# Performance work log

Measured on AMD Instinct MI355X. Metric: run time of the kernel, lower is better.

## Reference

```python
import jax, jax.numpy as jnp
import numpy as np


def setup_inputs() -> dict:
    key = jax.random.key(0)
    k1, k2, k3, k4, k5 = jax.random.split(key, 5)
    b, n, L, D, m = 8, 8192, 512, 128, 16
    x = jax.random.normal(k1, (b, n, L), dtype=jnp.float32)
    # attention MLP: Linear(L->D, no bias), Tanh, Linear(D->1, no bias)
    W1 = jax.random.normal(k2, (L, D), dtype=jnp.float32) / np.sqrt(L).astype(np.float32)
    W2 = jax.random.normal(k3, (D, 1), dtype=jnp.float32) / np.sqrt(D).astype(np.float32)
    batched_image_ids = jax.random.randint(k4, (b, n), 0, m)  # which image each packed token belongs to
    key_pad_mask = jax.random.bernoulli(k5, 0.1, (b, n))      # True = padding token
    return {"x": x, "W1": W1, "W2": W2,
            "batched_image_ids": batched_image_ids,
            "key_pad_mask": key_pad_mask,
            "max_queries": 16}


def reference(x, W1, W2, batched_image_ids, key_pad_mask, max_queries):
    # Attention scores per token: tanh(x W1) W2 -> [b, n, 1]
    A = jnp.tanh(x @ W1) @ W2
    A = jnp.swapaxes(A, -1, -2)  # [b, 1, n]
    b, n, d = x.shape
    # Per-image pooling mask: token j contributes to query i iff its image id == i and not padded
    image_id_arange = jnp.arange(max_queries)                                    # [m]
    attn_pool_mask = (image_id_arange[None, :, None] == batched_image_ids[:, None, :])
    attn_pool_mask = attn_pool_mask & (~key_pad_mask)[:, None, :]                # [b, m, n]
    neg = -jnp.finfo(A.dtype).max
    A = jnp.where(attn_pool_mask, jnp.broadcast_to(A, (b, max_queries, n)), neg)
    A = jax.nn.softmax(A, axis=-1)                                               # [b, m, n]
    out = jnp.einsum('bmn,bnd->bmd', A, x)                                       # pooled per image
    # num_images == max_queries for every bag -> is_images selects everything
    out = out.reshape(b * max_queries, d)
    return out
```

## Files before the change

kernel.cpp:

```cpp
#include <hip/hip_runtime.h>
#include <hip/hip_bf16.h>
#include <cstdint>
#include <cstddef>

typedef __attribute__((ext_vector_type(8))) short bf16x8;
typedef __attribute__((ext_vector_type(4))) float f32x4;

#define BATCH 8
#define NTOK 8192
#define LDIM 512
#define DDIM 128
#define NQ 16
#define NSEG 8
#define SEGLEN (NTOK / NSEG)

static __device__ __forceinline__ short f2bf(float f) {
  uint32_t u = __float_as_uint(f);
  uint32_t r = u + 0x7fffu + ((u >> 16) & 1u);
  return (short)(r >> 16);
}

static __device__ __forceinline__ bf16x8 cvt8(float4 a, float4 b) {
  bf16x8 o;
  o[0] = f2bf(a.x); o[1] = f2bf(a.y); o[2] = f2bf(a.z); o[3] = f2bf(a.w);
  o[4] = f2bf(b.x); o[5] = f2bf(b.y); o[6] = f2bf(b.z); o[7] = f2bf(b.w);
  return o;
}

static __device__ __forceinline__ unsigned int flipf(float v) {
  unsigned int u = __float_as_uint(v);
  return (u & 0x80000000u) ? ~u : (u | 0x80000000u);
}
static __device__ __forceinline__ float unflipf(unsigned int u) {
  return __uint_as_float((u & 0x80000000u) ? (u & 0x7fffffffu) : ~u);
}

static __device__ __forceinline__ bool is_pad(const void* pad, int byteFlag, int j) {
  return byteFlag ? (((const unsigned char*)pad)[j] != 0)
                  : (((const int*)pad)[j] != 0);
}

__global__ __launch_bounds__(256) void k0_wfrag(const float* __restrict__ W1,
                                                short* __restrict__ wfrag,
                                                const unsigned int* __restrict__ pad_raw,
                                                int* __restrict__ flag,
                                                unsigned int* __restrict__ gmax) {
  int tid = blockIdx.x * blockDim.x + threadIdx.x;
  if (tid < 16 * 8 * 64) {
    int l = tid & 63;
    int t = (tid >> 6) & 7;
    int c = tid >> 9;
    int kbase = c * 32 + (l >> 4) * 8;
    int col = t * 16 + (l & 15);
    bf16x8 frag;
#pragma unroll
    for (int i = 0; i < 8; ++i) frag[i] = f2bf(W1[(size_t)(kbase + i) * DDIM + col]);
    ((bf16x8*)wfrag)[tid] = frag;
  }
  if (blockIdx.x == 0) {
    if (threadIdx.x < 128) gmax[threadIdx.x] = 0u;
    int any_gt1 = 0;
    for (int i = threadIdx.x; i < 16384; i += 256)
      if (pad_raw[i] > 1u) any_gt1 = 1;
    unsigned long long m = __ballot(any_gt1);
    __shared__ int s[4];
    if ((threadIdx.x & 63) == 0) s[threadIdx.x >> 6] = (m != 0ull) ? 1 : 0;
    __syncthreads();
    if (threadIdx.x == 0) flag[0] = (s[0] | s[1] | s[2] | s[3]);
  }
}

__global__ __launch_bounds__(512, 6) void k1_scores(const float* __restrict__ x,
                                                    const short* __restrict__ wfrag,
                                                    const float* __restrict__ W2,
                                                    const int* __restrict__ ids,
                                                    const void* __restrict__ pad,
                                                    const int* __restrict__ flag,
                                                    float* __restrict__ A,
                                                    unsigned int* __restrict__ gmax) {
  __shared__ short ldsw[16384];
  __shared__ unsigned int qmax[16];
  const int tid = threadIdx.x, wave = tid >> 6, lane = tid & 63;
  const int rowBase = blockIdx.x * 128 + wave * 16;
  const int b = rowBase >> 13;
  const float* xp = x + (size_t)(rowBase + (lane & 15)) * LDIM + ((lane >> 4) * 8);
  if (tid < 16) qmax[tid] = 0u;

#define STAGE(qd)                                                                             \
  {                                                                                           \
    const unsigned int* src_ = (const unsigned int*)wfrag + (qd) * 8192;                      \
    _Pragma("unroll")                                                                         \
    for (int i = 0; i < 4; ++i) {                                                             \
      __builtin_amdgcn_global_load_lds(                                                       \
          (const __attribute__((address_space(1))) unsigned int*)(src_ + (i * 512 + tid) * 4),\
          (__attribute__((address_space(3))) unsigned int*)&ldsw[(i * 512 + wave * 64) * 8],  \
          16, 0, 0);                                                                          \
    }                                                                                         \
  }

#define ALOAD(dst, c)                                  \
  {                                                    \
    dst[0] = *(const float4*)(xp + (c) * 32);          \
    dst[1] = *(const float4*)(xp + (c) * 32 + 4);      \
  }

  f32x4 acc[8];
#pragma unroll
  for (int t = 0; t < 8; ++t) acc[t] = (f32x4){0.f, 0.f, 0.f, 0.f};
  float4 avbuf[2][2];

  STAGE(0);
  ALOAD(avbuf[0], 0);
  ALOAD(avbuf[1], 1);
  __syncthreads();

#pragma unroll
  for (int qd = 0; qd < 4; ++qd) {
#pragma unroll
    for (int cc = 0; cc < 4; ++cc) {
      const int c = qd * 4 + cc;
      bf16x8 af = cvt8(avbuf[c & 1][0], avbuf[c & 1][1]);
      if (c < 14) ALOAD(avbuf[c & 1], c + 2);
#pragma unroll
      for (int t = 0; t < 8; ++t) {
        bf16x8 bfr = *(const bf16x8*)&ldsw[((cc * 8 + t) * 64 + lane) * 8];
        acc[t] = __builtin_amdgcn_mfma_f32_16x16x32_bf16(af, bfr, acc[t], 0, 0, 0);
      }
    }
    if (qd < 3) {
      __syncthreads();
      STAGE(qd + 1);
      __syncthreads();
    }
  }
#undef STAGE
#undef ALOAD

  float w2v[8];
#pragma unroll
  for (int t = 0; t < 8; ++t) w2v[t] = W2[t * 16 + (lane & 15)];
  const int bfl = flag[0];
  float asum[4] = {0.f, 0.f, 0.f, 0.f};
#pragma unroll
  for (int t = 0; t < 8; ++t) {
#pragma unroll
    for (int r = 0; r < 4; ++r) {
      float h = 1.f - 2.f / (__expf(2.f * acc[t][r]) + 1.f);
      asum[r] += h * w2v[t];
    }
  }
#pragma unroll
  for (int m = 1; m < 16; m <<= 1) {
#pragma unroll
    for (int r = 0; r < 4; ++r) asum[r] += __shfl_xor(asum[r], m, 64);
  }
  if ((lane & 15) == 0) {
    int rb = rowBase + (lane >> 4) * 4;
#pragma unroll
    for (int r = 0; r < 4; ++r) {
      int row = rb + r;
      float v = asum[r];
      A[row] = v;
      if (!is_pad(pad, bfl, row)) atomicMax(&qmax[ids[row]], flipf(v));
    }
  }
  __syncthreads();
  if (tid < 16 && qmax[tid] != 0u) atomicMax(&gmax[(b << 4) + tid], qmax[tid]);
}

__global__ __launch_bounds__(256) void k3_pool(const float* __restrict__ x,
                                               const float* __restrict__ A,
                                               const int* __restrict__ ids,
                                               const void* __restrict__ pad,
                                               const int* __restrict__ flag,
                                               const unsigned int* __restrict__ gmax,
                                               float* __restrict__ partial,
                                               float* __restrict__ wsum) {
  int blk = blockIdx.x;
  int s = blk & 7, q = (blk >> 3) & 15, b = blk >> 7;
  int wave = threadIdx.x >> 6, lane = threadIdx.x & 63;
  int bfl = flag[0];
  __shared__ float w_u[1024];
  __shared__ unsigned short j_u[1024];
  __shared__ int cnt[4];
  __shared__ float wred[4];

  unsigned int mraw = gmax[(b << 4) + q];
  float mx = (mraw == 0u) ? 0.f : unflipf(mraw);
  const int base = b * NTOK;
  const int tokBase = s * SEGLEN + wave * 256;

  int myCnt = 0;
#pragma unroll
  for (int g = 0; g < 4; ++g) {
    int j = tokBase + g * 64 + lane;
    bool mem = (ids[base + j] == q) && !is_pad(pad, bfl, base + j);
    myCnt += __popcll(__ballot(mem));
  }
  if (lane == 0) cnt[wave] = myCnt;
  __syncthreads();

  int wpos = 0;
#pragma unroll
  for (int w = 0; w < 4; ++w) if (w < wave) wpos += cnt[w];
  const int total = cnt[0] + cnt[1] + cnt[2] + cnt[3];

  float wacc = 0.f;
#pragma unroll
  for (int g = 0; g < 4; ++g) {
    int j = tokBase + g * 64 + lane;
    bool mem = (ids[base + j] == q) && !is_pad(pad, bfl, base + j);
    float wt = mem ? __expf(A[base + j] - mx) : 0.f;
    wacc += wt;
    unsigned long long mask = __ballot(mem);
    if (mem) {
      int pos = wpos + __popcll(mask & ((1ull << lane) - 1ull));
      w_u[pos] = wt;
      j_u[pos] = (unsigned short)j;
    }
    wpos += __popcll(mask);
  }
#pragma unroll
  for (int m = 1; m < 64; m <<= 1) wacc += __shfl_xor(wacc, m, 64);
  if (lane == 0) wred[wave] = wacc;
  __syncthreads();

  int grp = threadIdx.x >> 7, ct = threadIdx.x & 127;
  int c0 = ct * 4;
  int half = (total + 1) >> 1;
  int e0 = grp ? half : 0;
  int e1 = grp ? total : half;
  float4 av = {0.f, 0.f, 0.f, 0.f};
  for (int e = e0; e < e1; ++e) {
    float wt = w_u[e];
    int j = j_u[e];
    float4 xr = *(const float4*)(x + (size_t)(base + j) * LDIM + c0);
    av.x += wt * xr.x; av.y += wt * xr.y; av.z += wt * xr.z; av.w += wt * xr.w;
  }
  *(float4*)(partial + ((size_t)(blk * 2 + grp)) * LDIM + c0) = av;
  if (threadIdx.x == 0) wsum[blk] = wred[0] + wred[1] + wred[2] + wred[3];
}

__global__ void k4_reduce(const float* __restrict__ partial, const float* __restrict__ wsum,
                          float* __restrict__ out) {
  int e = blockIdx.x * blockDim.x + threadIdx.x;
  if (e >= BATCH * NQ * LDIM) return;
  int bi = e >> 9, c = e & 511;
  float ps = 0.f, ws = 0.f;
#pragma unroll
  for (int t = 0; t < 16; ++t) ps += partial[(size_t)(bi * 16 + t) * LDIM + c];
#pragma unroll
  for (int t = 0; t < 8; ++t) ws += wsum[bi * 8 + t];
  out[e] = (ws > 0.f) ? (ps / ws) : 0.f;
}

extern "C" void kernel_launch(void* const* d_in, const int* in_sizes, int n_in,
                              void* d_out, int out_size, void* d_ws, size_t ws_size,
                              hipStream_t stream) {
  const float* x = (const float*)d_in[0];
  const float* W1 = (const float*)d_in[1];
  const float* W2 = (const float*)d_in[2];
  const int* ids = (const int*)d_in[3];
  const void* pad = d_in[4];
  float* out = (float*)d_out;

  char* ws = (char*)d_ws;
  short* wfrag = (short*)ws;
  float* A = (float*)(ws + 131072);
  unsigned int* gmax = (unsigned int*)(ws + 393216);
  float* wsum = (float*)(ws + 393728);
  int* flag = (int*)(ws + 397824);
  float* partial = (float*)(ws + 397952);

  hipLaunchKernelGGL(k0_wfrag, dim3(32), dim3(256), 0, stream,
                     W1, wfrag, (const unsigned int*)pad, flag, gmax);
  hipLaunchKernelGGL(k1_scores, dim3((BATCH * NTOK) / 128), dim3(512), 0, stream,
                     x, wfrag, W2, ids, pad, flag, A, gmax);
  hipLaunchKernelGGL(k3_pool, dim3(BATCH * NQ * NSEG), dim3(256), 0, stream,
                     x, A, ids, pad, flag, gmax, partial, wsum);
  hipLaunchKernelGGL(k4_reduce, dim3((BATCH * NQ * LDIM) / 256), dim3(256), 0, stream,
                     partial, wsum, out);
}
```

Before: 70.67 us.

## Fuse softmax-weighted pooling into score kernel, drop max pass and pool kernel

Computes exp of the attention score directly in the scores kernel and pools x rows of the same 128-token tile per image into per-block partials. This removes the separate pool kernel, so x is not read from memory a second time, and removes the global max atomics. The max subtraction is dropped, relying on the scores being bounded by the tanh. A larger partial buffer (16 per block) must now be written and reduced by a new reduce kernel.

New measurement: 91.90 us. 1.3x slower.

```diff
diff --git a/kernel.cpp b/kernel.cpp
--- a/kernel.cpp
+++ b/kernel.cpp
@@ -11,8 +11,6 @@
 #define LDIM 512
 #define DDIM 128
 #define NQ 16
-#define NSEG 8
-#define SEGLEN (NTOK / NSEG)
 
 static __device__ __forceinline__ short f2bf(float f) {
   uint32_t u = __float_as_uint(f);
@@ -27,14 +25,6 @@
   return o;
 }
 
-static __device__ __forceinline__ unsigned int flipf(float v) {
-  unsigned int u = __float_as_uint(v);
-  return (u & 0x80000000u) ? ~u : (u | 0x80000000u);
-}
-static __device__ __forceinline__ float unflipf(unsigned int u) {
-  return __uint_as_float((u & 0x80000000u) ? (u & 0x7fffffffu) : ~u);
-}
-
 static __device__ __forceinline__ bool is_pad(const void* pad, int byteFlag, int j) {
   return byteFlag ? (((const unsigned char*)pad)[j] != 0)
                   : (((const int*)pad)[j] != 0);
@@ -43,8 +33,7 @@
 __global__ __launch_bounds__(256) void k0_wfrag(const float* __restrict__ W1,
                                                 short* __restrict__ wfrag,
                                                 const unsigned int* __restrict__ pad_raw,
-                                                int* __restrict__ flag,
-                                                unsigned int* __restrict__ gmax) {
+                                                int* __restrict__ flag) {
   int tid = blockIdx.x * blockDim.x + threadIdx.x;
   if (tid < 16 * 8 * 64) {
     int l = tid & 63;
@@ -58,7 +47,6 @@
     ((bf16x8*)wfrag)[tid] = frag;
   }
   if (blockIdx.x == 0) {
-    if (threadIdx.x < 128) gmax[threadIdx.x] = 0u;
     int any_gt1 = 0;
     for (int i = threadIdx.x; i < 16384; i += 256)
       if (pad_raw[i] > 1u) any_gt1 = 1;
@@ -70,21 +58,22 @@
   }
 }
 
-__global__ __launch_bounds__(512, 6) void k1_scores(const float* __restrict__ x,
-                                                    const short* __restrict__ wfrag,
-                                                    const float* __restrict__ W2,
-                                                    const int* __restrict__ ids,
-                                                    const void* __restrict__ pad,
-                                                    const int* __restrict__ flag,
-                                                    float* __restrict__ A,
-                                                    unsigned int* __restrict__ gmax) {
+__global__ __launch_bounds__(512, 6) void k1_fused(const float* __restrict__ x,
+                                                   const short* __restrict__ wfrag,
+                                                   const float* __restrict__ W2,
+                                                   const int* __restrict__ ids,
+                                                   const void* __restrict__ pad,
+                                                   const int* __restrict__ flag,
+                                                   float* __restrict__ partial,
+                                                   float* __restrict__ wsum_p) {
   __shared__ short ldsw[16384];
-  __shared__ unsigned int qmax[16];
+  __shared__ float wt_l[128];
+  __shared__ int qq_l[128];
+  __shared__ int idx_l[128];
+  __shared__ int off_l[17];
   const int tid = threadIdx.x, wave = tid >> 6, lane = tid & 63;
   const int rowBase = blockIdx.x * 128 + wave * 16;
-  const int b = rowBase >> 13;
   const float* xp = x + (size_t)(rowBase + (lane & 15)) * LDIM + ((lane >> 4) * 8);
-  if (tid < 16) qmax[tid] = 0u;
 
 #define STAGE(qd)                                                                             \
   {                                                                                           \
@@ -155,103 +144,72 @@
     for (int r = 0; r < 4; ++r) asum[r] += __shfl_xor(asum[r], m, 64);
   }
   if ((lane & 15) == 0) {
-    int rb = rowBase + (lane >> 4) * 4;
 #pragma unroll
     for (int r = 0; r < 4; ++r) {
-      int row = rb + r;
-      float v = asum[r];
-      A[row] = v;
-      if (!is_pad(pad, bfl, row)) atomicMax(&qmax[ids[row]], flipf(v));
-    }
-  }
-  __syncthreads();
-  if (tid < 16 && qmax[tid] != 0u) atomicMax(&gmax[(b << 4) + tid], qmax[tid]);
-}
-
-__global__ __launch_bounds__(256) void k3_pool(const float* __restrict__ x,
-                                               const float* __restrict__ A,
-                                               const int* __restrict__ ids,
-                                               const void* __restrict__ pad,
-                                               const int* __restrict__ flag,
-                                               const unsigned int* __restrict__ gmax,
-                                               float* __restrict__ partial,
-                                               float* __restrict__ wsum) {
-  int blk = blockIdx.x;
-  int s = blk & 7, q = (blk >> 3) & 15, b = blk >> 7;
-  int wave = threadIdx.x >> 6, lane = threadIdx.x & 63;
-  int bfl = flag[0];
-  __shared__ float w_u[1024];
-  __shared__ unsigned short j_u[1024];
-  __shared__ int cnt[4];
-  __shared__ float wred[4];
-
-  unsigned int mraw = gmax[(b << 4) + q];
-  float mx = (mraw == 0u) ? 0.f : unflipf(mraw);
-  const int base = b * NTOK;
-  const int tokBase = s * SEGLEN + wave * 256;
-
-  int myCnt = 0;
-#pragma unroll
-  for (int g = 0; g < 4; ++g) {
-    int j = tokBase + g * 64 + lane;
-    bool mem = (ids[base + j] == q) && !is_pad(pad, bfl, base + j);
-    myCnt += __popcll(__ballot(mem));
-  }
-  if (lane == 0) cnt[wave] = myCnt;
-  __syncthreads();
-
-  int wpos = 0;
-#pragma unroll
-  for (int w = 0; w < 4; ++w) if (w < wave) wpos += cnt[w];
-  const int total = cnt[0] + cnt[1] + cnt[2] + cnt[3];
-
-  float wacc = 0.f;
-#pragma unroll
-  for (int g = 0; g < 4; ++g) {
-    int j = tokBase + g * 64 + lane;
-    bool mem = (ids[base + j] == q) && !is_pad(pad, bfl, base + j);
-    float wt = mem ? __expf(A[base + j] - mx) : 0.f;
-    wacc += wt;
-    unsigned long long mask = __ballot(mem);
-    if (mem) {
-      int pos = wpos + __popcll(mask & ((1ull << lane) - 1ull));
-      w_u[pos] = wt;
-      j_u[pos] = (unsigned short)j;
-    }
-    wpos += __popcll(mask);
-  }
-#pragma unroll
-  for (int m = 1; m < 64; m <<= 1) wacc += __shfl_xor(wacc, m, 64);
-  if (lane == 0) wred[wave] = wacc;
-  __syncthreads();
-
-  int grp = threadIdx.x >> 7, ct = threadIdx.x & 127;
-  int c0 = ct * 4;
-  int half = (total + 1) >> 1;
-  int e0 = grp ? half : 0;
-  int e1 = grp ? total : half;
-  float4 av = {0.f, 0.f, 0.f, 0.f};
-  for (int e = e0; e < e1; ++e) {
-    float wt = w_u[e];
-    int j = j_u[e];
-    float4 xr = *(const float4*)(x + (size_t)(base + j) * LDIM + c0);
-    av.x += wt * xr.x; av.y += wt * xr.y; av.z += wt * xr.z; av.w += wt * xr.w;
-  }
-  *(float4*)(partial + ((size_t)(blk * 2 + grp)) * LDIM + c0) = av;
-  if (threadIdx.x == 0) wsum[blk] = wred[0] + wred[1] + wred[2] + wred[3];
-}
-
-__global__ void k4_reduce(const float* __restrict__ partial, const float* __restrict__ wsum,
-                          float* __restrict__ out) {
-  int e = blockIdx.x * blockDim.x + threadIdx.x;
-  if (e >= BATCH * NQ * LDIM) return;
-  int bi = e >> 9, c = e & 511;
-  float ps = 0.f, ws = 0.f;
-#pragma unroll
-  for (int t = 0; t < 16; ++t) ps += partial[(size_t)(bi * 16 + t) * LDIM + c];
-#pragma unroll
-  for (int t = 0; t < 8; ++t) ws += wsum[bi * 8 + t];
-  out[e] = (ws > 0.f) ? (ps / ws) : 0.f;
+      int lr = wave * 16 + (lane >> 4) * 4 + r;
+      int row = blockIdx.x * 128 + lr;
+      wt_l[lr] = __expf(asum[r]);
+      qq_l[lr] = is_pad(pad, bfl, row) ? 16 : ids[row];
+    }
+  }
+  __syncthreads();
+
+  if (wave == 0) {
+    int q0 = qq_l[lane], q1 = qq_l[64 + lane];
+    unsigned long long below = (1ull << lane) - 1ull;
+    int pos = 0;
+    for (int q = 0; q < 16; ++q) {
+      if (lane == 0) off_l[q] = pos;
+      unsigned long long m0 = __ballot(q0 == q);
+      if (q0 == q) idx_l[pos + __popcll(m0 & below)] = lane;
+      int c0 = __popcll(m0);
+      unsigned long long m1 = __ballot(q1 == q);
+      if (q1 == q) idx_l[pos + c0 + __popcll(m1 & below)] = 64 + lane;
+      pos += c0 + __popcll(m1);
+    }
+    if (lane == 0) off_l[16] = pos;
+  }
+  __syncthreads();
+
+  if (tid < 16) {
+    float s = 0.f;
+    for (int e = off_l[tid]; e < off_l[tid + 1]; ++e) s += wt_l[idx_l[e]];
+    wsum_p[blockIdx.x * 16 + tid] = s;
+  }
+
+  const float* xc = x + (size_t)(blockIdx.x * 128) * LDIM + (wave * 64 + lane);
+  float* pb = partial + ((size_t)blockIdx.x * 16) * 512 + (wave * 64 + lane);
+#pragma unroll
+  for (int q = 0; q < 16; ++q) {
+    int e0 = off_l[q], e1 = off_l[q + 1];
+    float a = 0.f;
+    for (int e = e0; e < e1; ++e) {
+      int r = idx_l[e];
+      a = fmaf(wt_l[r], xc[(size_t)r * LDIM], a);
+    }
+    pb[(size_t)q * 512] = a;
+  }
+}
+
+__global__ __launch_bounds__(512) void k4_reduce(const float* __restrict__ partial,
+                                                 const float* __restrict__ wsum_p,
+                                                 float* __restrict__ out) {
+  int b = blockIdx.x >> 4, q = blockIdx.x & 15;
+  int tid = threadIdx.x;
+  __shared__ float wsh;
+  if (tid < 64) {
+    float v = wsum_p[(b * 64 + tid) * 16 + q];
+#pragma unroll
+    for (int m = 1; m < 64; m <<= 1) v += __shfl_xor(v, m, 64);
+    if (tid == 0) wsh = v;
+  }
+  __syncthreads();
+  float ws = wsh;
+  const float* pp = partial + ((size_t)(b * 64) * 16 + q) * 512 + tid;
+  float ps = 0.f;
+#pragma unroll 4
+  for (int t = 0; t < 64; ++t) ps += pp[(size_t)t * 16 * 512];
+  out[blockIdx.x * 512 + tid] = (ws > 0.f) ? (ps / ws) : 0.f;
 }
 
 extern "C" void kernel_launch(void* const* d_in, const int* in_sizes, int n_in,
@@ -266,18 +224,14 @@
 
   char* ws = (char*)d_ws;
   short* wfrag = (short*)ws;
-  float* A = (float*)(ws + 131072);
-  unsigned int* gmax = (unsigned int*)(ws + 393216);
-  float* wsum = (float*)(ws + 393728);
-  int* flag = (int*)(ws + 397824);
-  float* partial = (float*)(ws + 397952);
+  int* flag = (int*)(ws + 131072);
+  float* wsum_p = (float*)(ws + 131200);
+  float* partial = (float*)(ws + 262144);
 
   hipLaunchKernelGGL(k0_wfrag, dim3(32), dim3(256), 0, stream,
-                     W1, wfrag, (const unsigned int*)pad, flag, gmax);
-  hipLaunchKernelGGL(k1_scores, dim3((BATCH * NTOK) / 128), dim3(512), 0, stream,
-                     x, wfrag, W2, ids, pad, flag, A, gmax);
-  hipLaunchKernelGGL(k3_pool, dim3(BATCH * NQ * NSEG), dim3(256), 0, stream,
-                     x, A, ids, pad, flag, gmax, partial, wsum);
-  hipLaunchKernelGGL(k4_reduce, dim3((BATCH * NQ * LDIM) / 256), dim3(256), 0, stream,
-                     partial, wsum, out);
-}
+                     W1, wfrag, (const unsigned int*)pad, flag);
+  hipLaunchKernelGGL(k1_fused, dim3((BATCH * NTOK) / 128), dim3(512), 0, stream,
+                     x, wfrag, W2, ids, pad, flag, partial, wsum_p);
+  hipLaunchKernelGGL(k4_reduce, dim3(BATCH * NQ), dim3(512), 0, stream,
+                     partial, wsum_p, out);
+}
```

## Drop softmax max tracking, store exp scores, widen pooling blocks and prefetch

Applied to the files above, without the earlier changes.

The per-image running max (LDS and global atomics on flipped floats) is removed; the score kernel writes exp(score) directly, relying on scores staying small (|A| is bounded by the W2 norm since tanh lies in [-1,1]). This removes the atomics, the ids/pad reads in the score kernel and the gmax initialization. The score kernel also deepens the x prefetch from 2 to 4 chunks. The pooling kernel moves to 512 threads with 4 token groups and software-prefetched gathered rows, and the final reduction gets one block per (batch, query). The risk is overflow in exp without max subtraction, which the bounded scores make unlikely, plus higher register use from the deeper prefetch.

Result: faster. 66.58 us (-5.8%).

```diff
diff --git a/kernel.cpp b/kernel.cpp
--- a/kernel.cpp
+++ b/kernel.cpp
@@ -27,14 +27,6 @@
   return o;
 }
 
-static __device__ __forceinline__ unsigned int flipf(float v) {
-  unsigned int u = __float_as_uint(v);
-  return (u & 0x80000000u) ? ~u : (u | 0x80000000u);
-}
-static __device__ __forceinline__ float unflipf(unsigned int u) {
-  return __uint_as_float((u & 0x80000000u) ? (u & 0x7fffffffu) : ~u);
-}
-
 static __device__ __forceinline__ bool is_pad(const void* pad, int byteFlag, int j) {
   return byteFlag ? (((const unsigned char*)pad)[j] != 0)
                   : (((const int*)pad)[j] != 0);
@@ -43,8 +35,7 @@
 __global__ __launch_bounds__(256) void k0_wfrag(const float* __restrict__ W1,
                                                 short* __restrict__ wfrag,
                                                 const unsigned int* __restrict__ pad_raw,
-                                                int* __restrict__ flag,
-                                                unsigned int* __restrict__ gmax) {
+                                                int* __restrict__ flag) {
   int tid = blockIdx.x * blockDim.x + threadIdx.x;
   if (tid < 16 * 8 * 64) {
     int l = tid & 63;
@@ -58,7 +49,6 @@
     ((bf16x8*)wfrag)[tid] = frag;
   }
   if (blockIdx.x == 0) {
-    if (threadIdx.x < 128) gmax[threadIdx.x] = 0u;
     int any_gt1 = 0;
     for (int i = threadIdx.x; i < 16384; i += 256)
       if (pad_raw[i] > 1u) any_gt1 = 1;
@@ -73,18 +63,11 @@
 __global__ __launch_bounds__(512, 6) void k1_scores(const float* __restrict__ x,
                                                     const short* __restrict__ wfrag,
                                                     const float* __restrict__ W2,
-                                                    const int* __restrict__ ids,
-                                                    const void* __restrict__ pad,
-                                                    const int* __restrict__ flag,
-                                                    float* __restrict__ A,
-                                                    unsigned int* __restrict__ gmax) {
+                                                    float* __restrict__ expw) {
   __shared__ short ldsw[16384];
-  __shared__ unsigned int qmax[16];
   const int tid = threadIdx.x, wave = tid >> 6, lane = tid & 63;
   const int rowBase = blockIdx.x * 128 + wave * 16;
-  const int b = rowBase >> 13;
   const float* xp = x + (size_t)(rowBase + (lane & 15)) * LDIM + ((lane >> 4) * 8);
-  if (tid < 16) qmax[tid] = 0u;
 
 #define STAGE(qd)                                                                             \
   {                                                                                           \
@@ -107,11 +90,13 @@
   f32x4 acc[8];
 #pragma unroll
   for (int t = 0; t < 8; ++t) acc[t] = (f32x4){0.f, 0.f, 0.f, 0.f};
-  float4 avbuf[2][2];
+  float4 avbuf[4][2];
 
   STAGE(0);
   ALOAD(avbuf[0], 0);
   ALOAD(avbuf[1], 1);
+  ALOAD(avbuf[2], 2);
+  ALOAD(avbuf[3], 3);
   __syncthreads();
 
 #pragma unroll
@@ -119,8 +104,8 @@
 #pragma unroll
     for (int cc = 0; cc < 4; ++cc) {
       const int c = qd * 4 + cc;
-      bf16x8 af = cvt8(avbuf[c & 1][0], avbuf[c & 1][1]);
-      if (c < 14) ALOAD(avbuf[c & 1], c + 2);
+      bf16x8 af = cvt8(avbuf[c & 3][0], avbuf[c & 3][1]);
+      if (c < 12) ALOAD(avbuf[c & 3], c + 4);
 #pragma unroll
       for (int t = 0; t < 8; ++t) {
         bf16x8 bfr = *(const bf16x8*)&ldsw[((cc * 8 + t) * 64 + lane) * 8];
@@ -139,7 +124,6 @@
   float w2v[8];
 #pragma unroll
   for (int t = 0; t < 8; ++t) w2v[t] = W2[t * 16 + (lane & 15)];
-  const int bfl = flag[0];
   float asum[4] = {0.f, 0.f, 0.f, 0.f};
 #pragma unroll
   for (int t = 0; t < 8; ++t) {
@@ -157,23 +141,15 @@
   if ((lane & 15) == 0) {
     int rb = rowBase + (lane >> 4) * 4;
 #pragma unroll
-    for (int r = 0; r < 4; ++r) {
-      int row = rb + r;
-      float v = asum[r];
-      A[row] = v;
-      if (!is_pad(pad, bfl, row)) atomicMax(&qmax[ids[row]], flipf(v));
-    }
-  }
-  __syncthreads();
-  if (tid < 16 && qmax[tid] != 0u) atomicMax(&gmax[(b << 4) + tid], qmax[tid]);
-}
-
-__global__ __launch_bounds__(256) void k3_pool(const float* __restrict__ x,
-                                               const float* __restrict__ A,
+    for (int r = 0; r < 4; ++r) expw[rb + r] = __expf(asum[r]);
+  }
+}
+
+__global__ __launch_bounds__(512) void k3_pool(const float* __restrict__ x,
+                                               const float* __restrict__ expw,
                                                const int* __restrict__ ids,
                                                const void* __restrict__ pad,
                                                const int* __restrict__ flag,
-                                               const unsigned int* __restrict__ gmax,
                                                float* __restrict__ partial,
                                                float* __restrict__ wsum) {
   int blk = blockIdx.x;
@@ -182,17 +158,15 @@
   int bfl = flag[0];
   __shared__ float w_u[1024];
   __shared__ unsigned short j_u[1024];
-  __shared__ int cnt[4];
-  __shared__ float wred[4];
-
-  unsigned int mraw = gmax[(b << 4) + q];
-  float mx = (mraw == 0u) ? 0.f : unflipf(mraw);
+  __shared__ int cnt[8];
+  __shared__ float wred[8];
+
   const int base = b * NTOK;
-  const int tokBase = s * SEGLEN + wave * 256;
+  const int tokBase = s * SEGLEN + wave * 128;
 
   int myCnt = 0;
 #pragma unroll
-  for (int g = 0; g < 4; ++g) {
+  for (int g = 0; g < 2; ++g) {
     int j = tokBase + g * 64 + lane;
     bool mem = (ids[base + j] == q) && !is_pad(pad, bfl, base + j);
     myCnt += __popcll(__ballot(mem));
@@ -202,15 +176,15 @@
 
   int wpos = 0;
 #pragma unroll
-  for (int w = 0; w < 4; ++w) if (w < wave) wpos += cnt[w];
-  const int total = cnt[0] + cnt[1] + cnt[2] + cnt[3];
+  for (int w = 0; w < 8; ++w) if (w < wave) wpos += cnt[w];
+  const int total = cnt[0] + cnt[1] + cnt[2] + cnt[3] + cnt[4] + cnt[5] + cnt[6] + cnt[7];
 
   float wacc = 0.f;
 #pragma unroll
-  for (int g = 0; g < 4; ++g) {
+  for (int g = 0; g < 2; ++g) {
     int j = tokBase + g * 64 + lane;
     bool mem = (ids[base + j] == q) && !is_pad(pad, bfl, base + j);
-    float wt = mem ? __expf(A[base + j] - mx) : 0.f;
+    float wt = mem ? expw[base + j] : 0.f;
     wacc += wt;
     unsigned long long mask = __ballot(mem);
     if (mem) {
@@ -227,31 +201,45 @@
 
   int grp = threadIdx.x >> 7, ct = threadIdx.x & 127;
   int c0 = ct * 4;
-  int half = (total + 1) >> 1;
-  int e0 = grp ? half : 0;
-  int e1 = grp ? total : half;
+  int per = (total + 3) >> 2;
+  int e0 = grp * per;
+  int e1 = e0 + per; if (e1 > total) e1 = total;
   float4 av = {0.f, 0.f, 0.f, 0.f};
-  for (int e = e0; e < e1; ++e) {
+  if (e0 < e1) {
+    float4 cur = *(const float4*)(x + (size_t)(base + j_u[e0]) * LDIM + c0);
+    int e = e0;
+    for (; e + 1 < e1; ++e) {
+      float4 nxt = *(const float4*)(x + (size_t)(base + j_u[e + 1]) * LDIM + c0);
+      float wt = w_u[e];
+      av.x = fmaf(wt, cur.x, av.x); av.y = fmaf(wt, cur.y, av.y);
+      av.z = fmaf(wt, cur.z, av.z); av.w = fmaf(wt, cur.w, av.w);
+      cur = nxt;
+    }
     float wt = w_u[e];
-    int j = j_u[e];
-    float4 xr = *(const float4*)(x + (size_t)(base + j) * LDIM + c0);
-    av.x += wt * xr.x; av.y += wt * xr.y; av.z += wt * xr.z; av.w += wt * xr.w;
-  }
-  *(float4*)(partial + ((size_t)(blk * 2 + grp)) * LDIM + c0) = av;
-  if (threadIdx.x == 0) wsum[blk] = wred[0] + wred[1] + wred[2] + wred[3];
-}
-
-__global__ void k4_reduce(const float* __restrict__ partial, const float* __restrict__ wsum,
-                          float* __restrict__ out) {
-  int e = blockIdx.x * blockDim.x + threadIdx.x;
-  if (e >= BATCH * NQ * LDIM) return;
-  int bi = e >> 9, c = e & 511;
-  float ps = 0.f, ws = 0.f;
-#pragma unroll
-  for (int t = 0; t < 16; ++t) ps += partial[(size_t)(bi * 16 + t) * LDIM + c];
-#pragma unroll
-  for (int t = 0; t < 8; ++t) ws += wsum[bi * 8 + t];
-  out[e] = (ws > 0.f) ? (ps / ws) : 0.f;
+    av.x = fmaf(wt, cur.x, av.x); av.y = fmaf(wt, cur.y, av.y);
+    av.z = fmaf(wt, cur.z, av.z); av.w = fmaf(wt, cur.w, av.w);
+  }
+  *(float4*)(partial + ((size_t)(blk * 4 + grp)) * LDIM + c0) = av;
+  if (threadIdx.x == 0)
+    wsum[blk] = wred[0] + wred[1] + wred[2] + wred[3] + wred[4] + wred[5] + wred[6] + wred[7];
+}
+
+__global__ __launch_bounds__(512) void k4_reduce(const float* __restrict__ partial,
+                                                 const float* __restrict__ wsum,
+                                                 float* __restrict__ out) {
+  int bq = blockIdx.x;
+  int b = bq >> 4, q = bq & 15;
+  int c = threadIdx.x;
+  float ws = 0.f;
+#pragma unroll
+  for (int s = 0; s < 8; ++s) ws += wsum[b * 128 + q * 8 + s];
+  float ps = 0.f;
+#pragma unroll
+  for (int s = 0; s < 8; ++s)
+#pragma unroll
+    for (int g = 0; g < 4; ++g)
+      ps += partial[((size_t)((b * 128 + q * 8 + s) * 4 + g)) * LDIM + c];
+  out[bq * 512 + c] = (ws > 0.f) ? (ps / ws) : 0.f;
 }
 
 extern "C" void kernel_launch(void* const* d_in, const int* in_sizes, int n_in,
@@ -266,18 +254,17 @@
 
   char* ws = (char*)d_ws;
   short* wfrag = (short*)ws;
-  float* A = (float*)(ws + 131072);
-  unsigned int* gmax = (unsigned int*)(ws + 393216);
-  float* wsum = (float*)(ws + 393728);
-  int* flag = (int*)(ws + 397824);
-  float* partial = (float*)(ws + 397952);
+  int* flag = (int*)(ws + 131072);
+  float* expw = (float*)(ws + 131200);
+  float* wsum = (float*)(ws + 393344);
+  float* partial = (float*)(ws + 397440);
 
   hipLaunchKernelGGL(k0_wfrag, dim3(32), dim3(256), 0, stream,
-                     W1, wfrag, (const unsigned int*)pad, flag, gmax);
+                     W1, wfrag, (const unsigned int*)pad, flag);
   hipLaunchKernelGGL(k1_scores, dim3((BATCH * NTOK) / 128), dim3(512), 0, stream,
-                     x, wfrag, W2, ids, pad, flag, A, gmax);
-  hipLaunchKernelGGL(k3_pool, dim3(BATCH * NQ * NSEG), dim3(256), 0, stream,
-                     x, A, ids, pad, flag, gmax, partial, wsum);
-  hipLaunchKernelGGL(k4_reduce, dim3((BATCH * NQ * LDIM) / 256), dim3(256), 0, stream,
+                     x, wfrag, W2, expw);
+  hipLaunchKernelGGL(k3_pool, dim3(BATCH * NQ * NSEG), dim3(512), 0, stream,
+                     x, expw, ids, pad, flag, partial, wsum);
+  hipLaunchKernelGGL(k4_reduce, dim3(BATCH * NQ), dim3(512), 0, stream,
                      partial, wsum, out);
 }
```
